# Kernel tuning notes

Hardware: AMD Instinct MI355X
Metric: run time of the kernel (lower is better)

Reference implementation:

```python
import jax, jax.numpy as jnp
import numpy as np

NUM_HEADS = 8
SPARSITY = 0.7


def setup_inputs() -> dict:
    key = jax.random.key(0)
    k1, k2, k3, k4, k5 = jax.random.split(key, 5)
    B, N, C = 4, 2048, 256
    return {
        "x": jax.random.normal(k1, (B, N, C), dtype=jnp.float32),
        "w_qkv": jax.random.normal(k2, (3 * C, C), dtype=jnp.float32) * (C ** -0.5),
        "b_qkv": jax.random.normal(k3, (3 * C,), dtype=jnp.float32) * 0.02,
        "w_proj": jax.random.normal(k4, (C, C), dtype=jnp.float32) * (C ** -0.5),
        "b_proj": jax.random.normal(k5, (C,), dtype=jnp.float32) * 0.02,
    }


def reference(x, w_qkv, b_qkv, w_proj, b_proj):
    B, N, C = x.shape
    H = NUM_HEADS
    D = C // H
    scale = D ** -0.5
    # qkv projection (torch Linear: x @ W.T + b)
    qkv = x @ w_qkv.T + b_qkv                      # [B, N, 3C]
    qkv = qkv.reshape(B, N, 3, H, D).transpose(2, 0, 3, 1, 4)  # [3, B, H, N, D]
    q, k, v = qkv[0], qkv[1], qkv[2]
    attn = jnp.einsum('bhnd,bhmd->bhnm', q, k) * scale  # [B, H, N, N]
    # dynamic per-row top-k threshold mask (note: zeros out logits, not -inf,
    # faithfully matching the original torch code)
    num_keep = int(N * (1.0 - SPARSITY))
    topk_vals = jax.lax.top_k(attn, num_keep)[0]        # [B, H, N, num_keep]
    threshold = topk_vals[..., -1:]                      # k-th largest per row
    mask = (attn >= threshold).astype(attn.dtype)
    attn = attn * mask
    attn = jax.nn.softmax(attn, axis=-1)
    out = jnp.einsum('bhnm,bhmd->bhnd', attn, v)         # [B, H, N, D]
    out = out.transpose(0, 2, 1, 3).reshape(B, N, C)
    return out @ w_proj.T + b_proj
```

## Files before the change

kernel.cpp:

```cpp
#include <hip/hip_runtime.h>

#define BDIM 4
#define NSEQ 2048
#define CDIM 256
#define NHEADS 8
#define QB 4
#define NT2 32
#define NKEEP 614
#define SSTR 2056
#define ATTN_SCALE 0.17677669529663688f

__global__ __launch_bounds__(256) void gemm_nt_bias(
    const float* __restrict__ A, const float* __restrict__ W,
    const float* __restrict__ bias, float* __restrict__ C,
    int M, int Nt, int K)
{
    __shared__ __align__(16) float As[32][68];
    __shared__ __align__(16) float Ws[32][68];
    const int tid = threadIdx.x;
    const int bm = blockIdx.x * 64;
    const int bn = blockIdx.y * 64;
    const int tm = tid >> 4;
    const int tn = tid & 15;
    const int lr = tid >> 2;
    const int lq = tid & 3;
    const float* Ap = A + (size_t)(bm + lr) * K + lq * 8;
    const float* Wp = W + (size_t)(bn + lr) * K + lq * 8;
    float acc[4][4] = {};

    for (int k0 = 0; k0 < K; k0 += 32) {
        float4 a0 = *(const float4*)(Ap + k0);
        float4 a1 = *(const float4*)(Ap + k0 + 4);
        float4 w0 = *(const float4*)(Wp + k0);
        float4 w1 = *(const float4*)(Wp + k0 + 4);
        __syncthreads();
        const int kq = lq * 8;
        As[kq+0][lr]=a0.x; As[kq+1][lr]=a0.y; As[kq+2][lr]=a0.z; As[kq+3][lr]=a0.w;
        As[kq+4][lr]=a1.x; As[kq+5][lr]=a1.y; As[kq+6][lr]=a1.z; As[kq+7][lr]=a1.w;
        Ws[kq+0][lr]=w0.x; Ws[kq+1][lr]=w0.y; Ws[kq+2][lr]=w0.z; Ws[kq+3][lr]=w0.w;
        Ws[kq+4][lr]=w1.x; Ws[kq+5][lr]=w1.y; Ws[kq+6][lr]=w1.z; Ws[kq+7][lr]=w1.w;
        __syncthreads();
        #pragma unroll
        for (int k = 0; k < 32; ++k) {
            float4 av = *(const float4*)&As[k][tm*4];
            float4 wv = *(const float4*)&Ws[k][tn*4];
            acc[0][0] += av.x*wv.x; acc[0][1] += av.x*wv.y; acc[0][2] += av.x*wv.z; acc[0][3] += av.x*wv.w;
            acc[1][0] += av.y*wv.x; acc[1][1] += av.y*wv.y; acc[1][2] += av.y*wv.z; acc[1][3] += av.y*wv.w;
            acc[2][0] += av.z*wv.x; acc[2][1] += av.z*wv.y; acc[2][2] += av.z*wv.z; acc[2][3] += av.z*wv.w;
            acc[3][0] += av.w*wv.x; acc[3][1] += av.w*wv.y; acc[3][2] += av.w*wv.z; acc[3][3] += av.w*wv.w;
        }
    }
    float4 bb = *(const float4*)(bias + bn + tn*4);
    #pragma unroll
    for (int i = 0; i < 4; ++i) {
        float4 o;
        o.x = acc[i][0] + bb.x;
        o.y = acc[i][1] + bb.y;
        o.z = acc[i][2] + bb.z;
        o.w = acc[i][3] + bb.w;
        *(float4*)(C + (size_t)(bm + tm*4 + i) * Nt + bn + tn*4) = o;
    }
}

__device__ __forceinline__ unsigned int f2key(float f) {
    unsigned int u = __float_as_uint(f);
    return (u & 0x80000000u) ? ~u : (u | 0x80000000u);
}
__device__ __forceinline__ float dpp_xor1_add(float x) {
    int s = __builtin_amdgcn_mov_dpp(__float_as_int(x), 0xB1, 0xF, 0xF, true);
    return x + __int_as_float(s);
}
__device__ __forceinline__ float dpp_xor2_add(float x) {
    int s = __builtin_amdgcn_mov_dpp(__float_as_int(x), 0x4E, 0xF, 0xF, true);
    return x + __int_as_float(s);
}

#define RBAR() do { asm volatile("s_waitcnt lgkmcnt(0)" ::: "memory"); \
                    __builtin_amdgcn_s_barrier();                      \
                    asm volatile("" ::: "memory"); } while (0)
#define LGKM0() asm volatile("s_waitcnt lgkmcnt(0)" ::: "memory")

__global__ __launch_bounds__(256, 4) void sparse_attn(
    const float* __restrict__ qkv, float* __restrict__ aout)
{
    __shared__ __align__(16) float  sbuf[QB * SSTR];
    __shared__ __align__(16) unsigned int hist[QB * 256];
    __shared__ unsigned int prefS[QB];
    __shared__ int   remS[QB];
    __shared__ float zS[QB];

    const int tid = threadIdx.x;
    const int w   = tid >> 6;
    const int l   = tid & 63;
    const int p   = l & 3;
    const int jg  = l >> 2;

    const int blk = blockIdx.x;
    const int nqb = NSEQ / QB;
    const int bh  = blk / nqb;
    const int qblk = blk % nqb;
    const int b = bh / NHEADS, h = bh % NHEADS;
    const int n0 = qblk * QB;

    const float* base = qkv + (size_t)b * NSEQ * 768;
    const float* kptr = base + 256 + h * 32 + p * 4 + (size_t)((w << 9) + jg) * 768;
    const float* vptr = base + 512 + h * 32 + p * 4 + (size_t)((w << 9) + jg) * 768;
#define KADDR(t) (kptr + (size_t)(t) * (16 * 768))
#define VADDR(t) (vptr + (size_t)(t) * (16 * 768))

    float4 qa[QB], qc[QB];
    {
        const float* gq = base + (size_t)n0 * 768 + h * 32 + p * 4;
        #pragma unroll
        for (int r = 0; r < QB; ++r) {
            float4 x0 = *(const float4*)(gq + (size_t)r * 768);
            float4 x1 = *(const float4*)(gq + (size_t)r * 768 + 16);
            qa[r].x = x0.x * ATTN_SCALE; qa[r].y = x0.y * ATTN_SCALE;
            qa[r].z = x0.z * ATTN_SCALE; qa[r].w = x0.w * ATTN_SCALE;
            qc[r].x = x1.x * ATTN_SCALE; qc[r].y = x1.y * ATTN_SCALE;
            qc[r].z = x1.z * ATTN_SCALE; qc[r].w = x1.w * ATTN_SCALE;
        }
    }
    {
        uint4 z4; z4.x = 0u; z4.y = 0u; z4.z = 0u; z4.w = 0u;
        *(uint4*)(hist + tid * 4) = z4;
    }
    if (tid < QB) { prefS[tid] = 0u; remS[tid] = NKEEP; }
    RBAR();

#define QK_TILE(K0, K1, T) do {                                               \
        float sc0 = qa[0].x*(K0).x + qa[0].y*(K0).y + qa[0].z*(K0).z + qa[0].w*(K0).w \
                  + qc[0].x*(K1).x + qc[0].y*(K1).y + qc[0].z*(K1).z + qc[0].w*(K1).w; \
        float sc1 = qa[1].x*(K0).x + qa[1].y*(K0).y + qa[1].z*(K0).z + qa[1].w*(K0).w \
                  + qc[1].x*(K1).x + qc[1].y*(K1).y + qc[1].z*(K1).z + qc[1].w*(K1).w; \
        float sc2 = qa[2].x*(K0).x + qa[2].y*(K0).y + qa[2].z*(K0).z + qa[2].w*(K0).w \
                  + qc[2].x*(K1).x + qc[2].y*(K1).y + qc[2].z*(K1).z + qc[2].w*(K1).w; \
        float sc3 = qa[3].x*(K0).x + qa[3].y*(K0).y + qa[3].z*(K0).z + qa[3].w*(K0).w \
                  + qc[3].x*(K1).x + qc[3].y*(K1).y + qc[3].z*(K1).z + qc[3].w*(K1).w; \
        sc0 = dpp_xor2_add(dpp_xor1_add(sc0));                                \
        sc1 = dpp_xor2_add(dpp_xor1_add(sc1));                                \
        sc2 = dpp_xor2_add(dpp_xor1_add(sc2));                                \
        sc3 = dpp_xor2_add(dpp_xor1_add(sc3));                                \
        float myv = (p == 0) ? sc0 : (p == 1) ? sc1 : (p == 2) ? sc2 : sc3;   \
        const int col = (w << 9) + ((T) << 4) + jg;                           \
        sbuf[p * SSTR + col] = myv;                                           \
        atomicAdd(&hist[p * 256 + (f2key(myv) >> 24)], 1u);                   \
    } while (0)

    float4 ka0 = *(const float4*)(KADDR(0)), ka1 = *(const float4*)(KADDR(0) + 16);
    float4 kb0 = *(const float4*)(KADDR(1)), kb1 = *(const float4*)(KADDR(1) + 16);
    float4 kc0 = *(const float4*)(KADDR(2)), kc1 = *(const float4*)(KADDR(2) + 16);
    float4 kd0 = *(const float4*)(KADDR(3)), kd1 = *(const float4*)(KADDR(3) + 16);
    #pragma unroll 1
    for (int t = 0; t < NT2; t += 4) {
        float4 c0, c1;
        c0 = ka0; c1 = ka1;
        if (t + 4 < NT2) { ka0 = *(const float4*)(KADDR(t + 4)); ka1 = *(const float4*)(KADDR(t + 4) + 16); }
        QK_TILE(c0, c1, t);
        c0 = kb0; c1 = kb1;
        if (t + 5 < NT2) { kb0 = *(const float4*)(KADDR(t + 5)); kb1 = *(const float4*)(KADDR(t + 5) + 16); }
        QK_TILE(c0, c1, t + 1);
        c0 = kc0; c1 = kc1;
        if (t + 6 < NT2) { kc0 = *(const float4*)(KADDR(t + 6)); kc1 = *(const float4*)(KADDR(t + 6) + 16); }
        QK_TILE(c0, c1, t + 2);
        c0 = kd0; c1 = kd1;
        if (t + 7 < NT2) { kd0 = *(const float4*)(KADDR(t + 7)); kd1 = *(const float4*)(KADDR(t + 7) + 16); }
        QK_TILE(c0, c1, t + 3);
    }
    float4 va0 = *(const float4*)(VADDR(0)), va1 = *(const float4*)(VADDR(0) + 16);
    float4 vb0 = *(const float4*)(VADDR(1)), vb1 = *(const float4*)(VADDR(1) + 16);
    float4 vc0 = *(const float4*)(VADDR(2)), vc1 = *(const float4*)(VADDR(2) + 16);
    float4 vd0 = *(const float4*)(VADDR(3)), vd1 = *(const float4*)(VADDR(3) + 16);
    RBAR();

    unsigned int* hrow = hist + w * 256;
    #pragma unroll 1
    for (int pass = 3; pass >= 0; --pass) {
        const int sh = pass * 8;
        const unsigned int pr = prefS[w];
        const int remv = remS[w];
        if (pass != 3) {
            const unsigned int hmsk = 0xFFFFFFFFu << (sh + 8);
            uint4 z4; z4.x = 0u; z4.y = 0u; z4.z = 0u; z4.w = 0u;
            *(uint4*)(hrow + l * 4) = z4;
            LGKM0();
            #pragma unroll 2
            for (int e = 0; e < 8; ++e) {
                float4 v = *(const float4*)&sbuf[w * SSTR + l * 4 + 256 * e];
                unsigned int k0 = f2key(v.x), k1 = f2key(v.y), k2 = f2key(v.z), k3 = f2key(v.w);
                if ((k0 & hmsk) == pr) atomicAdd(&hrow[(k0 >> sh) & 255u], 1u);
                if ((k1 & hmsk) == pr) atomicAdd(&hrow[(k1 >> sh) & 255u], 1u);
                if ((k2 & hmsk) == pr) atomicAdd(&hrow[(k2 >> sh) & 255u], 1u);
                if ((k3 & hmsk) == pr) atomicAdd(&hrow[(k3 >> sh) & 255u], 1u);
            }
            LGKM0();
        }
        uint4 c4 = *(const uint4*)(hrow + l * 4);
        unsigned int cnt[4] = { c4.x, c4.y, c4.z, c4.w };
        unsigned int part = cnt[0] + cnt[1] + cnt[2] + cnt[3];
        unsigned int suf = part;
        #pragma unroll
        for (int dlt = 1; dlt < 64; dlt <<= 1) {
            unsigned int v = __shfl_down(suf, dlt);
            if (l + dlt < 64) suf += v;
        }
        unsigned int run = suf - part;
        #pragma unroll
        for (int i = 3; i >= 0; --i) {
            if ((int)run < remv && remv <= (int)(run + cnt[i])) {
                remS[w]  = remv - (int)run;
                prefS[w] = pr | ((unsigned int)(l * 4 + i) << sh);
            }
            run += cnt[i];
        }
        LGKM0();
    }

    {
        unsigned int key = prefS[w];
        unsigned int u = (key & 0x80000000u) ? (key & 0x7FFFFFFFu) : ~key;
        const float thr = __uint_as_float(u);
        float mx = 0.f;
        #pragma unroll 2
        for (int e = 0; e < 8; ++e) {
            float* sp = &sbuf[w * SSTR + l * 4 + 256 * e];
            float4 v = *(const float4*)sp;
            v.x = (v.x >= thr) ? v.x : 0.f;
            v.y = (v.y >= thr) ? v.y : 0.f;
            v.z = (v.z >= thr) ? v.z : 0.f;
            v.w = (v.w >= thr) ? v.w : 0.f;
            *(float4*)sp = v;
            mx = fmaxf(mx, fmaxf(fmaxf(v.x, v.y), fmaxf(v.z, v.w)));
        }
        #pragma unroll
        for (int d2 = 32; d2 >= 1; d2 >>= 1) mx = fmaxf(mx, __shfl_xor(mx, d2));
        float Z = 0.f;
        const float cm = __expf(0.f - mx);
        if (thr > 0.f) {
            #pragma unroll 2
            for (int e = 0; e < 8; ++e) {
                float* sp = &sbuf[w * SSTR + l * 4 + 256 * e];
                float4 v = *(const float4*)sp;
                v.x = (v.x > 0.f) ? __expf(v.x - mx) : cm;
                v.y = (v.y > 0.f) ? __expf(v.y - mx) : cm;
                v.z = (v.z > 0.f) ? __expf(v.z - mx) : cm;
                v.w = (v.w > 0.f) ? __expf(v.w - mx) : cm;
                *(float4*)sp = v;
                Z += v.x + v.y + v.z + v.w;
            }
        } else {
            #pragma unroll 2
            for (int e = 0; e < 8; ++e) {
                float* sp = &sbuf[w * SSTR + l * 4 + 256 * e];
                float4 v = *(const float4*)sp;
                v.x = __expf(v.x - mx); v.y = __expf(v.y - mx);
                v.z = __expf(v.z - mx); v.w = __expf(v.w - mx);
                *(float4*)sp = v;
                Z += v.x + v.y + v.z + v.w;
            }
        }
        #pragma unroll
        for (int d2 = 32; d2 >= 1; d2 >>= 1) Z += __shfl_xor(Z, d2);
        if (l == 0) zS[w] = Z;
    }
    RBAR();

    float4 oa0, oa1, oa2, oa3, ob0, ob1, ob2, ob3;
    oa0.x=0;oa0.y=0;oa0.z=0;oa0.w=0; ob0=oa0; oa1=oa0; ob1=oa0;
    oa2=oa0; ob2=oa0; oa3=oa0; ob3=oa0;

#define PV_TILE(V0, V1, T) do {                                               \
        const int col = (w << 9) + ((T) << 4) + jg;                           \
        float p0 = sbuf[0 * SSTR + col];                                      \
        float p1 = sbuf[1 * SSTR + col];                                      \
        float p2 = sbuf[2 * SSTR + col];                                      \
        float p3 = sbuf[3 * SSTR + col];                                      \
        oa0.x=fmaf(p0,(V0).x,oa0.x); oa0.y=fmaf(p0,(V0).y,oa0.y); oa0.z=fmaf(p0,(V0).z,oa0.z); oa0.w=fmaf(p0,(V0).w,oa0.w); \
        ob0.x=fmaf(p0,(V1).x,ob0.x); ob0.y=fmaf(p0,(V1).y,ob0.y); ob0.z=fmaf(p0,(V1).z,ob0.z); ob0.w=fmaf(p0,(V1).w,ob0.w); \
        oa1.x=fmaf(p1,(V0).x,oa1.x); oa1.y=fmaf(p1,(V0).y,oa1.y); oa1.z=fmaf(p1,(V0).z,oa1.z); oa1.w=fmaf(p1,(V0).w,oa1.w); \
        ob1.x=fmaf(p1,(V1).x,ob1.x); ob1.y=fmaf(p1,(V1).y,ob1.y); ob1.z=fmaf(p1,(V1).z,ob1.z); ob1.w=fmaf(p1,(V1).w,ob1.w); \
        oa2.x=fmaf(p2,(V0).x,oa2.x); oa2.y=fmaf(p2,(V0).y,oa2.y); oa2.z=fmaf(p2,(V0).z,oa2.z); oa2.w=fmaf(p2,(V0).w,oa2.w); \
        ob2.x=fmaf(p2,(V1).x,ob2.x); ob2.y=fmaf(p2,(V1).y,ob2.y); ob2.z=fmaf(p2,(V1).z,ob2.z); ob2.w=fmaf(p2,(V1).w,ob2.w); \
        oa3.x=fmaf(p3,(V0).x,oa3.x); oa3.y=fmaf(p3,(V0).y,oa3.y); oa3.z=fmaf(p3,(V0).z,oa3.z); oa3.w=fmaf(p3,(V0).w,oa3.w); \
        ob3.x=fmaf(p3,(V1).x,ob3.x); ob3.y=fmaf(p3,(V1).y,ob3.y); ob3.z=fmaf(p3,(V1).z,ob3.z); ob3.w=fmaf(p3,(V1).w,ob3.w); \
    } while (0)

    #pragma unroll 1
    for (int t = 0; t < NT2; t += 4) {
        float4 c0, c1;
        c0 = va0; c1 = va1;
        if (t + 4 < NT2) { va0 = *(const float4*)(VADDR(t + 4)); va1 = *(const float4*)(VADDR(t + 4) + 16); }
        PV_TILE(c0, c1, t);
        c0 = vb0; c1 = vb1;
        if (t + 5 < NT2) { vb0 = *(const float4*)(VADDR(t + 5)); vb1 = *(const float4*)(VADDR(t + 5) + 16); }
        PV_TILE(c0, c1, t + 1);
        c0 = vc0; c1 = vc1;
        if (t + 6 < NT2) { vc0 = *(const float4*)(VADDR(t + 6)); vc1 = *(const float4*)(VADDR(t + 6) + 16); }
        PV_TILE(c0, c1, t + 2);
        c0 = vd0; c1 = vd1;
        if (t + 7 < NT2) { vd0 = *(const float4*)(VADDR(t + 7)); vd1 = *(const float4*)(VADDR(t + 7) + 16); }
        PV_TILE(c0, c1, t + 3);
    }
    RBAR();

    #pragma unroll
    for (int d2 = 4; d2 <= 32; d2 <<= 1) {
        oa0.x+=__shfl_xor(oa0.x,d2); oa0.y+=__shfl_xor(oa0.y,d2); oa0.z+=__shfl_xor(oa0.z,d2); oa0.w+=__shfl_xor(oa0.w,d2);
        ob0.x+=__shfl_xor(ob0.x,d2); ob0.y+=__shfl_xor(ob0.y,d2); ob0.z+=__shfl_xor(ob0.z,d2); ob0.w+=__shfl_xor(ob0.w,d2);
        oa1.x+=__shfl_xor(oa1.x,d2); oa1.y+=__shfl_xor(oa1.y,d2); oa1.z+=__shfl_xor(oa1.z,d2); oa1.w+=__shfl_xor(oa1.w,d2);
        ob1.x+=__shfl_xor(ob1.x,d2); ob1.y+=__shfl_xor(ob1.y,d2); ob1.z+=__shfl_xor(ob1.z,d2); ob1.w+=__shfl_xor(ob1.w,d2);
        oa2.x+=__shfl_xor(oa2.x,d2); oa2.y+=__shfl_xor(oa2.y,d2); oa2.z+=__shfl_xor(oa2.z,d2); oa2.w+=__shfl_xor(oa2.w,d2);
        ob2.x+=__shfl_xor(ob2.x,d2); ob2.y+=__shfl_xor(ob2.y,d2); ob2.z+=__shfl_xor(ob2.z,d2); ob2.w+=__shfl_xor(ob2.w,d2);
        oa3.x+=__shfl_xor(oa3.x,d2); oa3.y+=__shfl_xor(oa3.y,d2); oa3.z+=__shfl_xor(oa3.z,d2); oa3.w+=__shfl_xor(oa3.w,d2);
        ob3.x+=__shfl_xor(ob3.x,d2); ob3.y+=__shfl_xor(ob3.y,d2); ob3.z+=__shfl_xor(ob3.z,d2); ob3.w+=__shfl_xor(ob3.w,d2);
    }
    if (l < 4) {
        float* part = &sbuf[0];
        *(float4*)&part[(w * 4 + 0) * 32 + l * 4]      = oa0;
        *(float4*)&part[(w * 4 + 0) * 32 + 16 + l * 4] = ob0;
        *(float4*)&part[(w * 4 + 1) * 32 + l * 4]      = oa1;
        *(float4*)&part[(w * 4 + 1) * 32 + 16 + l * 4] = ob1;
        *(float4*)&part[(w * 4 + 2) * 32 + l * 4]      = oa2;
        *(float4*)&part[(w * 4 + 2) * 32 + 16 + l * 4] = ob2;
        *(float4*)&part[(w * 4 + 3) * 32 + l * 4]      = oa3;
        *(float4*)&part[(w * 4 + 3) * 32 + 16 + l * 4] = ob3;
    }
    RBAR();
    if (tid < 128) {
        const int r = tid >> 5, d = tid & 31;
        const float* part = &sbuf[0];
        float o = part[(0 * 4 + r) * 32 + d] + part[(1 * 4 + r) * 32 + d]
                + part[(2 * 4 + r) * 32 + d] + part[(3 * 4 + r) * 32 + d];
        o /= zS[r];
        aout[((size_t)b * NSEQ + n0 + r) * CDIM + h * 32 + d] = o;
    }
}

extern "C" void kernel_launch(void* const* d_in, const int* in_sizes, int n_in,
                              void* d_out, int out_size, void* d_ws, size_t ws_size,
                              hipStream_t stream) {
    (void)in_sizes; (void)n_in; (void)out_size; (void)ws_size;
    const float* x      = (const float*)d_in[0];
    const float* w_qkv  = (const float*)d_in[1];
    const float* b_qkv  = (const float*)d_in[2];
    const float* w_proj = (const float*)d_in[3];
    const float* b_proj = (const float*)d_in[4];
    float* out = (float*)d_out;

    const int M = BDIM * NSEQ;
    float* qkv_ws  = (float*)d_ws;
    float* attn_ws = qkv_ws + (size_t)M * 768;

    dim3 g1(M / 64, 768 / 64);
    gemm_nt_bias<<<g1, 256, 0, stream>>>(x, w_qkv, b_qkv, qkv_ws, M, 768, 256);

    sparse_attn<<<BDIM * NHEADS * (NSEQ / QB), 256, 0, stream>>>(qkv_ws, attn_ws);

    dim3 g2(M / 64, 256 / 64);
    gemm_nt_bias<<<g2, 256, 0, stream>>>(attn_ws, w_proj, b_proj, out, M, 256, 256);
}
```

Measured before the change: 653.9 us.

## Compute QK scores with split-bf16 MFMA using pre-packed K

Adds a pack_k kernel that rewrites K in place as hi/lo bf16 pairs. The QK score loop now uses three bf16 MFMA 16x16x32 ops (hi*hi, hi*lo, lo*hi) instead of scalar FMAs with DPP reductions, which keeps accuracy close to fp32. The QB=4 query rows are padded to 16 rows, so 12 of 16 MFMA rows do no useful work. The change also adds an extra kernel launch and a full pass over K in memory, and only the score stage is affected, while top-k selection and PV are unchanged.

```diff
diff --git a/kernel.cpp b/kernel.cpp
--- a/kernel.cpp
+++ b/kernel.cpp
@@ -9,6 +9,9 @@
 #define NKEEP 614
 #define SSTR 2056
 #define ATTN_SCALE 0.17677669529663688f
+
+typedef __bf16 bf16x8 __attribute__((ext_vector_type(8)));
+typedef float  f32x4  __attribute__((ext_vector_type(4)));
 
 __global__ __launch_bounds__(256) void gemm_nt_bias(
     const float* __restrict__ A, const float* __restrict__ W,
@@ -62,23 +65,50 @@
     }
 }
 
+__global__ __launch_bounds__(256) void pack_k(float* __restrict__ qkv)
+{
+    const size_t i = (size_t)blockIdx.x * 256 + threadIdx.x;
+    const size_t row = i >> 6;
+    const int c4 = (int)(i & 63);
+    float* p = qkv + row * 768 + 256 + c4 * 4;
+    float4 v = *(const float4*)p;
+    float xs[4] = { v.x, v.y, v.z, v.w };
+    unsigned int o[4];
+    #pragma unroll
+    for (int j = 0; j < 4; ++j) {
+        float x = xs[j];
+        __bf16 hb = (__bf16)x;
+        __bf16 lb = (__bf16)(x - (float)hb);
+        o[j] = ((unsigned int)__builtin_bit_cast(unsigned short, hb) << 16)
+             |  (unsigned int)__builtin_bit_cast(unsigned short, lb);
+    }
+    uint4 w4; w4.x = o[0]; w4.y = o[1]; w4.z = o[2]; w4.w = o[3];
+    *(uint4*)p = w4;
+}
+
 __device__ __forceinline__ unsigned int f2key(float f) {
     unsigned int u = __float_as_uint(f);
     return (u & 0x80000000u) ? ~u : (u | 0x80000000u);
-}
-__device__ __forceinline__ float dpp_xor1_add(float x) {
-    int s = __builtin_amdgcn_mov_dpp(__float_as_int(x), 0xB1, 0xF, 0xF, true);
-    return x + __int_as_float(s);
-}
-__device__ __forceinline__ float dpp_xor2_add(float x) {
-    int s = __builtin_amdgcn_mov_dpp(__float_as_int(x), 0x4E, 0xF, 0xF, true);
-    return x + __int_as_float(s);
 }
 
 #define RBAR() do { asm volatile("s_waitcnt lgkmcnt(0)" ::: "memory"); \
                     __builtin_amdgcn_s_barrier();                      \
                     asm volatile("" ::: "memory"); } while (0)
 #define LGKM0() asm volatile("s_waitcnt lgkmcnt(0)" ::: "memory")
+
+#define UNPK(U0, U1, BH, BL) do {                                             \
+        uint4 hw_, lw_;                                                       \
+        hw_.x = __builtin_amdgcn_perm((U0).y, (U0).x, 0x07060302u);           \
+        lw_.x = __builtin_amdgcn_perm((U0).y, (U0).x, 0x05040100u);           \
+        hw_.y = __builtin_amdgcn_perm((U0).w, (U0).z, 0x07060302u);           \
+        lw_.y = __builtin_amdgcn_perm((U0).w, (U0).z, 0x05040100u);           \
+        hw_.z = __builtin_amdgcn_perm((U1).y, (U1).x, 0x07060302u);           \
+        lw_.z = __builtin_amdgcn_perm((U1).y, (U1).x, 0x05040100u);           \
+        hw_.w = __builtin_amdgcn_perm((U1).w, (U1).z, 0x07060302u);           \
+        lw_.w = __builtin_amdgcn_perm((U1).w, (U1).z, 0x05040100u);           \
+        BH = __builtin_bit_cast(bf16x8, hw_);                                 \
+        BL = __builtin_bit_cast(bf16x8, lw_);                                 \
+    } while (0)
 
 __global__ __launch_bounds__(256, 4) void sparse_attn(
     const float* __restrict__ qkv, float* __restrict__ aout)
@@ -103,22 +133,25 @@
     const int n0 = qblk * QB;
 
     const float* base = qkv + (size_t)b * NSEQ * 768;
-    const float* kptr = base + 256 + h * 32 + p * 4 + (size_t)((w << 9) + jg) * 768;
+    const float* kbase0 = base + 256 + h * 32 + (l >> 4) * 8
+                        + (size_t)((w << 9) + (l & 15)) * 768;
+#define KADDR(t) ((const unsigned int*)(kbase0 + (size_t)(t) * (16 * 768)))
     const float* vptr = base + 512 + h * 32 + p * 4 + (size_t)((w << 9) + jg) * 768;
-#define KADDR(t) (kptr + (size_t)(t) * (16 * 768))
 #define VADDR(t) (vptr + (size_t)(t) * (16 * 768))
 
-    float4 qa[QB], qc[QB];
+    bf16x8 ah, al;
     {
-        const float* gq = base + (size_t)n0 * 768 + h * 32 + p * 4;
-        #pragma unroll
-        for (int r = 0; r < QB; ++r) {
-            float4 x0 = *(const float4*)(gq + (size_t)r * 768);
-            float4 x1 = *(const float4*)(gq + (size_t)r * 768 + 16);
-            qa[r].x = x0.x * ATTN_SCALE; qa[r].y = x0.y * ATTN_SCALE;
-            qa[r].z = x0.z * ATTN_SCALE; qa[r].w = x0.w * ATTN_SCALE;
-            qc[r].x = x1.x * ATTN_SCALE; qc[r].y = x1.y * ATTN_SCALE;
-            qc[r].z = x1.z * ATTN_SCALE; qc[r].w = x1.w * ATTN_SCALE;
+        #pragma unroll
+        for (int j = 0; j < 8; ++j) { ah[j] = (__bf16)0.f; al[j] = (__bf16)0.f; }
+        if ((l & 15) < QB) {
+            const float* gq = base + (size_t)(n0 + (l & 15)) * 768 + h * 32 + (l >> 4) * 8;
+            #pragma unroll
+            for (int j = 0; j < 8; ++j) {
+                float x = gq[j] * ATTN_SCALE;
+                __bf16 hb = (__bf16)x;
+                ah[j] = hb;
+                al[j] = (__bf16)(x - (float)hb);
+            }
         }
     }
     {
@@ -128,44 +161,36 @@
     if (tid < QB) { prefS[tid] = 0u; remS[tid] = NKEEP; }
     RBAR();
 
-#define QK_TILE(K0, K1, T) do {                                               \
-        float sc0 = qa[0].x*(K0).x + qa[0].y*(K0).y + qa[0].z*(K0).z + qa[0].w*(K0).w \
-                  + qc[0].x*(K1).x + qc[0].y*(K1).y + qc[0].z*(K1).z + qc[0].w*(K1).w; \
-        float sc1 = qa[1].x*(K0).x + qa[1].y*(K0).y + qa[1].z*(K0).z + qa[1].w*(K0).w \
-                  + qc[1].x*(K1).x + qc[1].y*(K1).y + qc[1].z*(K1).z + qc[1].w*(K1).w; \
-        float sc2 = qa[2].x*(K0).x + qa[2].y*(K0).y + qa[2].z*(K0).z + qa[2].w*(K0).w \
-                  + qc[2].x*(K1).x + qc[2].y*(K1).y + qc[2].z*(K1).z + qc[2].w*(K1).w; \
-        float sc3 = qa[3].x*(K0).x + qa[3].y*(K0).y + qa[3].z*(K0).z + qa[3].w*(K0).w \
-                  + qc[3].x*(K1).x + qc[3].y*(K1).y + qc[3].z*(K1).z + qc[3].w*(K1).w; \
-        sc0 = dpp_xor2_add(dpp_xor1_add(sc0));                                \
-        sc1 = dpp_xor2_add(dpp_xor1_add(sc1));                                \
-        sc2 = dpp_xor2_add(dpp_xor1_add(sc2));                                \
-        sc3 = dpp_xor2_add(dpp_xor1_add(sc3));                                \
-        float myv = (p == 0) ? sc0 : (p == 1) ? sc1 : (p == 2) ? sc2 : sc3;   \
-        const int col = (w << 9) + ((T) << 4) + jg;                           \
-        sbuf[p * SSTR + col] = myv;                                           \
-        atomicAdd(&hist[p * 256 + (f2key(myv) >> 24)], 1u);                   \
+#define MFMA_TILE(U0, U1, T) do {                                             \
+        bf16x8 bh_, bl_;                                                      \
+        UNPK(U0, U1, bh_, bl_);                                               \
+        f32x4 acc_ = {0.f, 0.f, 0.f, 0.f};                                    \
+        acc_ = __builtin_amdgcn_mfma_f32_16x16x32_bf16(al, bh_, acc_, 0, 0, 0); \
+        acc_ = __builtin_amdgcn_mfma_f32_16x16x32_bf16(ah, bl_, acc_, 0, 0, 0); \
+        acc_ = __builtin_amdgcn_mfma_f32_16x16x32_bf16(ah, bh_, acc_, 0, 0, 0); \
+        if (l < 16) {                                                         \
+            const int col_ = (w << 9) + ((T) << 4) + l;                       \
+            sbuf[0 * SSTR + col_] = acc_[0];                                  \
+            sbuf[1 * SSTR + col_] = acc_[1];                                  \
+            sbuf[2 * SSTR + col_] = acc_[2];                                  \
+            sbuf[3 * SSTR + col_] = acc_[3];                                  \
+            atomicAdd(&hist[0 * 256 + (f2key(acc_[0]) >> 24)], 1u);           \
+            atomicAdd(&hist[1 * 256 + (f2key(acc_[1]) >> 24)], 1u);           \
+            atomicAdd(&hist[2 * 256 + (f2key(acc_[2]) >> 24)], 1u);           \
+            atomicAdd(&hist[3 * 256 + (f2key(acc_[3]) >> 24)], 1u);           \
+        }                                                                     \
     } while (0)
 
-    float4 ka0 = *(const float4*)(KADDR(0)), ka1 = *(const float4*)(KADDR(0) + 16);
-    float4 kb0 = *(const float4*)(KADDR(1)), kb1 = *(const float4*)(KADDR(1) + 16);
-    float4 kc0 = *(const float4*)(KADDR(2)), kc1 = *(const float4*)(KADDR(2) + 16);
-    float4 kd0 = *(const float4*)(KADDR(3)), kd1 = *(const float4*)(KADDR(3) + 16);
+    uint4 kua0 = *(const uint4*)(KADDR(0)), kua1 = *(const uint4*)(KADDR(0) + 4);
+    uint4 kub0 = *(const uint4*)(KADDR(1)), kub1 = *(const uint4*)(KADDR(1) + 4);
     #pragma unroll 1
-    for (int t = 0; t < NT2; t += 4) {
-        float4 c0, c1;
-        c0 = ka0; c1 = ka1;
-        if (t + 4 < NT2) { ka0 = *(const float4*)(KADDR(t + 4)); ka1 = *(const float4*)(KADDR(t + 4) + 16); }
-        QK_TILE(c0, c1, t);
-        c0 = kb0; c1 = kb1;
-        if (t + 5 < NT2) { kb0 = *(const float4*)(KADDR(t + 5)); kb1 = *(const float4*)(KADDR(t + 5) + 16); }
-        QK_TILE(c0, c1, t + 1);
-        c0 = kc0; c1 = kc1;
-        if (t + 6 < NT2) { kc0 = *(const float4*)(KADDR(t + 6)); kc1 = *(const float4*)(KADDR(t + 6) + 16); }
-        QK_TILE(c0, c1, t + 2);
-        c0 = kd0; c1 = kd1;
-        if (t + 7 < NT2) { kd0 = *(const float4*)(KADDR(t + 7)); kd1 = *(const float4*)(KADDR(t + 7) + 16); }
-        QK_TILE(c0, c1, t + 3);
+    for (int t = 0; t < NT2; t += 2) {
+        uint4 c0 = kua0, c1 = kua1;
+        if (t + 2 < NT2) { kua0 = *(const uint4*)(KADDR(t + 2)); kua1 = *(const uint4*)(KADDR(t + 2) + 4); }
+        MFMA_TILE(c0, c1, t);
+        uint4 d0 = kub0, d1 = kub1;
+        if (t + 3 < NT2) { kub0 = *(const uint4*)(KADDR(t + 3)); kub1 = *(const uint4*)(KADDR(t + 3) + 4); }
+        MFMA_TILE(d0, d1, t + 1);
     }
     float4 va0 = *(const float4*)(VADDR(0)), va1 = *(const float4*)(VADDR(0) + 16);
     float4 vb0 = *(const float4*)(VADDR(1)), vb1 = *(const float4*)(VADDR(1) + 16);
@@ -354,6 +379,8 @@
     dim3 g1(M / 64, 768 / 64);
     gemm_nt_bias<<<g1, 256, 0, stream>>>(x, w_qkv, b_qkv, qkv_ws, M, 768, 256);
 
+    pack_k<<<BDIM * NSEQ * 64 / 256, 256, 0, stream>>>(qkv_ws);
+
     sparse_attn<<<BDIM * NHEADS * (NSEQ / QB), 256, 0, stream>>>(qkv_ws, attn_ws);
 
     dim3 g2(M / 64, 256 / 64);
```

New measurement: 752.1 us (median of 2 runs). 15.0% more time.
